# Performance work log

Hardware: AMD Instinct MI355X
Metric: run time of the kernel (lower is better)

Reference implementation:

```python
import jax, jax.numpy as jnp
import numpy as np

B, S, D = 2, 1024, 2048
L = 4
HQ, HKV, HD = 32, 8, 64
I = 5632
V = 32000
EPS = 1e-5
THETA = 10000.0
SCALE = HD ** -0.5
GROUP = HQ // HKV


def setup_inputs() -> dict:
    key = jax.random.key(0)
    ks = jax.random.split(key, 8)
    s = 0.02
    return {
        "input_ids": jax.random.randint(ks[0], (B, S), 0, V, dtype=jnp.int32),
        "positions": jnp.broadcast_to(jnp.arange(S, dtype=jnp.int32), (B, S)),
        "embed": jax.random.normal(ks[1], (V, D), jnp.float32) * s,
        "w_qkv": jax.random.normal(ks[2], (L, D, (HQ + 2 * HKV) * HD), jnp.float32) * s,
        "w_o": jax.random.normal(ks[3], (L, HQ * HD, D), jnp.float32) * s,
        "w_gate_up": jax.random.normal(ks[4], (L, D, 2 * I), jnp.float32) * s,
        "w_down": jax.random.normal(ks[5], (L, I, D), jnp.float32) * s,
        "ln1_w": jnp.ones((L, D), jnp.float32),
        "ln2_w": jnp.ones((L, D), jnp.float32),
        "norm_w": jnp.ones((D,), jnp.float32),
    }


def rmsnorm(x, w):
    var = jnp.mean(x * x, axis=-1, keepdims=True)
    return x * jax.lax.rsqrt(var + EPS) * w


def rope(positions, x):
    # x: [B, S, H, HD]; neox-style rotate-half RoPE
    inv_freq = 1.0 / (THETA ** (jnp.arange(0, HD, 2, dtype=jnp.float32) / HD))
    ang = positions.astype(jnp.float32)[..., None] * inv_freq  # [B, S, HD/2]
    cos = jnp.cos(ang)[:, :, None, :]
    sin = jnp.sin(ang)[:, :, None, :]
    x1, x2 = jnp.split(x, 2, axis=-1)
    return jnp.concatenate([x1 * cos - x2 * sin, x2 * cos + x1 * sin], axis=-1)


def llama_forward(input_ids, positions, embed, w_qkv, w_o, w_gate_up, w_down,
                  ln1_w, ln2_w, norm_w):
    h = embed[input_ids]                      # [B, S, D]
    res = jnp.zeros_like(h)
    causal = jnp.tril(jnp.ones((S, S), dtype=bool))
    neg = jnp.asarray(jnp.finfo(h.dtype).min, h.dtype)

    def layer(carry, params):
        h, res = carry
        wqkv, wo, wgu, wd, l1, l2 = params
        # fused RMSNorm + residual-add (vllm RMSNorm(x, residual) semantics)
        res = h + res
        h = rmsnorm(res, l1)
        # QKV projection + RoPE
        qkv = h @ wqkv
        q, k, v = jnp.split(qkv, [HQ * HD, (HQ + HKV) * HD], axis=-1)
        q = q.reshape(B, S, HQ, HD)
        k = k.reshape(B, S, HKV, HD)
        v = v.reshape(B, S, HKV, HD)
        q = rope(positions, q)
        k = rope(positions, k)
        # GQA: broadcast kv heads across query groups
        k = jnp.repeat(k, GROUP, axis=2)      # [B, S, HQ, HD]
        v = jnp.repeat(v, GROUP, axis=2)
        scores = jnp.einsum('bqhd,bkhd->bhqk', q, k) * SCALE
        scores = jnp.where(causal, scores, neg)
        attn = jax.nn.softmax(scores, axis=-1)
        o = jnp.einsum('bhqk,bkhd->bqhd', attn, v).reshape(B, S, HQ * HD)
        h = o @ wo
        # post-attention fused RMSNorm + residual
        res = h + res
        h = rmsnorm(res, l2)
        # SwiGLU MLP
        gu = h @ wgu
        g, u = jnp.split(gu, 2, axis=-1)
        h = (jax.nn.silu(g) * u) @ wd
        return (h, res), None

    (h, res), _ = jax.lax.scan(layer, (h, res),
                               (w_qkv, w_o, w_gate_up, w_down, ln1_w, ln2_w))
    return rmsnorm(h + res, norm_w)


def reference(input_ids, positions, embed, w_qkv, w_o, w_gate_up, w_down,
              ln1_w, ln2_w, norm_w):
    return llama_forward(input_ids, positions, embed, w_qkv, w_o, w_gate_up,
                         w_down, ln1_w, ln2_w, norm_w)
```

## Files before the change

### kernel.cpp

```cpp
#include <hip/hip_runtime.h>
#include <hip/hip_bf16.h>

#define B_ 2
#define S_ 1024
#define T_ (B_*S_)
#define D_ 2048
#define L_ 4
#define HQ_ 32
#define HKV_ 8
#define HD_ 64
#define I_ 5632
#define EPS_ 1e-5f
#define SCALE_ 0.125f

typedef __attribute__((ext_vector_type(4))) float  float4v;
typedef __attribute__((ext_vector_type(8))) short  short8v;

#define GLOAD16(g, l) \
  __builtin_amdgcn_global_load_lds((const __attribute__((address_space(1))) void*)(g), \
                                   (__attribute__((address_space(3))) void*)(l), 16, 0, 0)

__device__ __forceinline__ short f2bf(float f) {
  union { float f; unsigned u; } c; c.f = f;
  unsigned u = c.u + 0x7fffu + ((c.u >> 16) & 1u);
  return (short)(u >> 16);
}

__device__ __forceinline__ void xcd_swizzle(int gx, int gy, int& bx, int& by) {
  int nwg = gx * gy;
  int orig = by * gx + bx;
  int q = nwg >> 3, r = nwg & 7;
  int xcd = orig & 7, loc = orig >> 3;
  int swz = (xcd < r ? xcd * (q + 1) : r * (q + 1) + (xcd - r) * q) + loc;
  bx = swz / gy;
  by = swz - bx * gy;
}

__global__ __launch_bounds__(256)
void transpose_bf16(const float* __restrict__ in, short* __restrict__ out,
                    int K, int N) {
  __shared__ float t[32][33];
  const int bx = blockIdx.x * 32;
  const int by = blockIdx.y * 32;
  const int tx = threadIdx.x, ty = threadIdx.y;
  #pragma unroll
  for (int j = 0; j < 32; j += 8)
    t[ty + j][tx] = in[(size_t)(by + ty + j) * N + bx + tx];
  __syncthreads();
  #pragma unroll
  for (int j = 0; j < 32; j += 8)
    out[(size_t)(bx + ty + j) * K + by + tx] = f2bf(t[tx][ty + j]);
}

__global__ __launch_bounds__(256)
void embed_gather(const int* __restrict__ ids, const float* __restrict__ embed,
                  float* __restrict__ h) {
  size_t i = (size_t)blockIdx.x * 256 + threadIdx.x;
  int t  = (int)(i >> 9);
  int d4 = (int)(i & 511);
  ((float4v*)h)[i] = ((const float4v*)(embed + (size_t)ids[t] * D_))[d4];
}

__global__ __launch_bounds__(256)
void rmsnorm_add(const float* __restrict__ x, float* __restrict__ res,
                 const float* __restrict__ w, void* __restrict__ outp,
                 int first, int bf16out) {
  const int row = blockIdx.x;
  const int tid = threadIdx.x;
  const size_t base = (size_t)row * D_;
  float4v v0 = ((const float4v*)(x + base))[tid * 2];
  float4v v1 = ((const float4v*)(x + base))[tid * 2 + 1];
  if (!first) {
    v0 += ((const float4v*)(res + base))[tid * 2];
    v1 += ((const float4v*)(res + base))[tid * 2 + 1];
  }
  ((float4v*)(res + base))[tid * 2]     = v0;
  ((float4v*)(res + base))[tid * 2 + 1] = v1;
  float ss = v0[0]*v0[0] + v0[1]*v0[1] + v0[2]*v0[2] + v0[3]*v0[3]
           + v1[0]*v1[0] + v1[1]*v1[1] + v1[2]*v1[2] + v1[3]*v1[3];
  #pragma unroll
  for (int off = 32; off > 0; off >>= 1) ss += __shfl_xor(ss, off, 64);
  __shared__ float red[4];
  if ((tid & 63) == 0) red[tid >> 6] = ss;
  __syncthreads();
  float tot = red[0] + red[1] + red[2] + red[3];
  float rs = rsqrtf(tot * (1.0f / D_) + EPS_);
  float4v w0 = ((const float4v*)w)[tid * 2];
  float4v w1 = ((const float4v*)w)[tid * 2 + 1];
  float4v o0 = v0 * rs * w0;
  float4v o1 = v1 * rs * w1;
  if (bf16out) {
    short8v y;
    #pragma unroll
    for (int k = 0; k < 4; k++) { y[k] = f2bf(o0[k]); y[k + 4] = f2bf(o1[k]); }
    ((short8v*)((char*)outp + base * 2))[tid] = y;
  } else {
    float* op = (float*)outp + base;
    ((float4v*)op)[tid * 2]     = o0;
    ((float4v*)op)[tid * 2 + 1] = o1;
  }
}

#define BM 128
#define BN 128
#define BKS 32

__global__ __launch_bounds__(256)
void gemm_n64(const short* __restrict__ A, const short* __restrict__ Bt,
              float* __restrict__ C, int M, int N, int K) {
  __shared__ short sA[BM * BKS];
  __shared__ short sB[64 * BKS];
  int bx = blockIdx.x, by = blockIdx.y;
  xcd_swizzle(gridDim.x, gridDim.y, bx, by);
  const int tid  = threadIdx.x;
  const int lane = tid & 63;
  const int wave = tid >> 6;
  const int wm = (wave >> 1) << 6;
  const int wn = (wave & 1) << 5;
  const int row0 = by * BM;
  const int col0 = bx * 64;
  const int fr = lane & 15;
  const int fk = (lane >> 4) << 3;
  float4v acc[4][2] = {};

  const int r_st  = tid >> 2;
  const int kc_st = (tid & 3) << 3;
  const short* pA = A  + (size_t)(row0 + r_st) * K + kc_st;
  const short* pB = Bt + (size_t)(col0 + r_st) * K + kc_st;
  const size_t stride64 = (size_t)64 * K;
  short* lA0 = &sA[tid * 8];
  short* lA1 = &sA[(256 + tid) * 8];
  short* lB0 = &sB[tid * 8];

  for (int k0 = 0; k0 < K; k0 += BKS) {
    GLOAD16(pA, lA0);
    GLOAD16(pA + stride64, lA1);
    GLOAD16(pB, lB0);
    pA += BKS; pB += BKS;
    __syncthreads();
    short8v af[4], bfr[2];
    #pragma unroll
    for (int f = 0; f < 4; f++)
      af[f] = *(const short8v*)(&sA[(wm + f * 16 + fr) * BKS + fk]);
    #pragma unroll
    for (int f = 0; f < 2; f++)
      bfr[f] = *(const short8v*)(&sB[(wn + f * 16 + fr) * BKS + fk]);
    #pragma unroll
    for (int i = 0; i < 4; i++)
      #pragma unroll
      for (int j = 0; j < 2; j++)
        acc[i][j] = __builtin_amdgcn_mfma_f32_16x16x32_bf16(af[i], bfr[j], acc[i][j], 0, 0, 0);
    __syncthreads();
  }
  const int cr = (lane >> 4) << 2;
  const int cc = lane & 15;
  #pragma unroll
  for (int i = 0; i < 4; i++)
    #pragma unroll
    for (int j = 0; j < 2; j++) {
      size_t base = (size_t)(row0 + wm + i * 16 + cr) * N + col0 + wn + j * 16 + cc;
      #pragma unroll
      for (int r = 0; r < 4; r++)
        C[base + (size_t)r * N] = acc[i][j][r];
    }
}

__global__ __launch_bounds__(256)
void gemm_glu(const short* __restrict__ A, const short* __restrict__ Bt,
              short* __restrict__ mlp, int K) {
  __shared__ short sA[BM * BKS];
  __shared__ short sG[64 * BKS];
  __shared__ short sU[64 * BKS];
  int bx = blockIdx.x, by = blockIdx.y;
  xcd_swizzle(gridDim.x, gridDim.y, bx, by);
  const int tid  = threadIdx.x;
  const int lane = tid & 63;
  const int wave = tid >> 6;
  const int wm = (wave >> 1) << 6;
  const int wn = (wave & 1) << 5;
  const int row0 = by * BM;
  const int col0 = bx * 64;
  const int fr = lane & 15;
  const int fk = (lane >> 4) << 3;
  float4v accg[4][2] = {};
  float4v accu[4][2] = {};

  const int r_st  = tid >> 2;
  const int kc_st = (tid & 3) << 3;
  const short* pA = A  + (size_t)(row0 + r_st) * K + kc_st;
  const short* pG = Bt + (size_t)(col0 + r_st) * K + kc_st;
  const short* pU = Bt + (size_t)(col0 + I_ + r_st) * K + kc_st;
  const size_t stride64 = (size_t)64 * K;
  short* lA0 = &sA[tid * 8];
  short* lA1 = &sA[(256 + tid) * 8];
  short* lG0 = &sG[tid * 8];
  short* lU0 = &sU[tid * 8];

  for (int k0 = 0; k0 < K; k0 += BKS) {
    GLOAD16(pA, lA0);
    GLOAD16(pA + stride64, lA1);
    GLOAD16(pG, lG0);
    GLOAD16(pU, lU0);
    pA += BKS; pG += BKS; pU += BKS;
    __syncthreads();
    short8v af[4], bg[2], bu[2];
    #pragma unroll
    for (int f = 0; f < 4; f++)
      af[f] = *(const short8v*)(&sA[(wm + f * 16 + fr) * BKS + fk]);
    #pragma unroll
    for (int f = 0; f < 2; f++) {
      bg[f] = *(const short8v*)(&sG[(wn + f * 16 + fr) * BKS + fk]);
      bu[f] = *(const short8v*)(&sU[(wn + f * 16 + fr) * BKS + fk]);
    }
    #pragma unroll
    for (int i = 0; i < 4; i++)
      #pragma unroll
      for (int j = 0; j < 2; j++) {
        accg[i][j] = __builtin_amdgcn_mfma_f32_16x16x32_bf16(af[i], bg[j], accg[i][j], 0, 0, 0);
        accu[i][j] = __builtin_amdgcn_mfma_f32_16x16x32_bf16(af[i], bu[j], accu[i][j], 0, 0, 0);
      }
    __syncthreads();
  }
  const int cr = (lane >> 4) << 2;
  const int cc = lane & 15;
  #pragma unroll
  for (int i = 0; i < 4; i++)
    #pragma unroll
    for (int j = 0; j < 2; j++) {
      size_t base = (size_t)(row0 + wm + i * 16 + cr) * I_ + col0 + wn + j * 16 + cc;
      #pragma unroll
      for (int r = 0; r < 4; r++) {
        float g = accg[i][j][r], u = accu[i][j][r];
        mlp[base + (size_t)r * I_] = f2bf(g / (1.0f + __expf(-g)) * u);
      }
    }
}

__global__ __launch_bounds__(256)
void gemm_qkv_rope(const short* __restrict__ A, const short* __restrict__ Bt,
                   const float* __restrict__ tab, short* __restrict__ qbf,
                   short* __restrict__ kbf, short* __restrict__ vbf, int K) {
  __shared__ short sA[BM * BKS];
  __shared__ short sB[BN * BKS];
  int bx = blockIdx.x, by = blockIdx.y;
  xcd_swizzle(gridDim.x, gridDim.y, bx, by);
  const int tid  = threadIdx.x;
  const int lane = tid & 63;
  const int wave = tid >> 6;
  const int wm = (wave >> 1) << 6;
  const int wn = (wave & 1) << 6;
  const int row0 = by * BM;
  const int col0 = bx * BN;
  const int fr = lane & 15;
  const int fk = (lane >> 4) << 3;
  float4v acc[4][4] = {};

  const int r_st  = tid >> 2;
  const int kc_st = (tid & 3) << 3;
  const short* pA = A  + (size_t)(row0 + r_st) * K + kc_st;
  const short* pB = Bt + (size_t)(col0 + r_st) * K + kc_st;
  const size_t stride64 = (size_t)64 * K;
  short* lA0 = &sA[tid * 8];
  short* lA1 = &sA[(256 + tid) * 8];
  short* lB0 = &sB[tid * 8];
  short* lB1 = &sB[(256 + tid) * 8];

  for (int k0 = 0; k0 < K; k0 += BKS) {
    GLOAD16(pA, lA0);
    GLOAD16(pA + stride64, lA1);
    GLOAD16(pB, lB0);
    GLOAD16(pB + stride64, lB1);
    pA += BKS; pB += BKS;
    __syncthreads();
    short8v af[4], bfr[4];
    #pragma unroll
    for (int f = 0; f < 4; f++) {
      af[f]  = *(const short8v*)(&sA[(wm + f * 16 + fr) * BKS + fk]);
      bfr[f] = *(const short8v*)(&sB[(wn + f * 16 + fr) * BKS + fk]);
    }
    #pragma unroll
    for (int i = 0; i < 4; i++)
      #pragma unroll
      for (int j = 0; j < 4; j++)
        acc[i][j] = __builtin_amdgcn_mfma_f32_16x16x32_bf16(af[i], bfr[j], acc[i][j], 0, 0, 0);
    __syncthreads();
  }
  const int cr = (lane >> 4) << 2;
  const int cc = lane & 15;
  const int head = (col0 + wn) >> 6;

  if (head < HQ_ + HKV_) {
    const float sc = (head < HQ_) ? SCALE_ : 1.0f;
    #pragma unroll
    for (int i = 0; i < 4; i++)
      #pragma unroll
      for (int jj = 0; jj < 2; jj++)
        #pragma unroll
        for (int r = 0; r < 4; r++) {
          int m = row0 + wm + i * 16 + cr + r;
          int b = m >> 10, s = m & (S_ - 1);
          int d1 = jj * 16 + cc;
          float x1 = acc[i][jj][r], x2 = acc[i][jj + 2][r];
          const float* tb = tab + (size_t)m * 64 + d1 * 2;
          float c = tb[0], sn = tb[1];
          short y1 = f2bf((x1 * c - x2 * sn) * sc);
          short y2 = f2bf((x2 * c + x1 * sn) * sc);
          size_t base;
          if (head < HQ_)
            base = ((size_t)((b * HQ_ + head) * S_ + s)) * HD_;
          else
            base = ((size_t)((b * HKV_ + head - HQ_) * S_ + s)) * HD_;
          short* dst = (head < HQ_) ? qbf : kbf;
          dst[base + d1]      = y1;
          dst[base + d1 + 32] = y2;
        }
  } else {
    const int vh = head - HQ_ - HKV_;
    #pragma unroll
    for (int i = 0; i < 4; i++)
      #pragma unroll
      for (int j = 0; j < 4; j++)
        #pragma unroll
        for (int r = 0; r < 4; r++) {
          int m = row0 + wm + i * 16 + cr + r;
          int b = m >> 10, s = m & (S_ - 1);
          vbf[((size_t)((b * HKV_ + vh) * S_ + s)) * HD_ + j * 16 + cc] =
              f2bf(acc[i][j][r]);
        }
  }
}

__global__ __launch_bounds__(256)
void rope_table(const int* __restrict__ pos, float* __restrict__ tab) {
  int i = blockIdx.x * 256 + threadIdx.x;
  int t = i >> 5, ii = i & 31;
  float p = (float)pos[t];
  float freq = __expf(-(float)ii * (9.210340371976184f / 32.0f));
  float ang = p * freq;
  tab[2 * i]     = cosf(ang);
  tab[2 * i + 1] = sinf(ang);
}

#define KPAD 68

__global__ __launch_bounds__(256)
void transpose_v(const short* __restrict__ vbf, short* __restrict__ vtbf) {
  __shared__ short sv[64 * KPAD];
  const int jt = blockIdx.x, kh = blockIdx.y, b = blockIdx.z;
  const int tid = threadIdx.x;
  const short* src = vbf + ((size_t)((b * HKV_ + kh) * S_ + jt * 64)) * HD_;
  #pragma unroll
  for (int it = 0; it < 2; it++) {
    int c = it * 256 + tid;
    int rr = c >> 3, ch = (c & 7) * 8;
    *(short8v*)(&sv[rr * KPAD + ch]) = *(const short8v*)(src + (size_t)rr * HD_ + ch);
  }
  __syncthreads();
  const int dc = tid >> 2;
  const int jc = (tid & 3) * 16;
  short8v o1, o2;
  #pragma unroll
  for (int k = 0; k < 8; k++) o1[k] = sv[(jc + k) * KPAD + dc];
  #pragma unroll
  for (int k = 0; k < 8; k++) o2[k] = sv[(jc + 8 + k) * KPAD + dc];
  short* od = vtbf + ((size_t)((b * HKV_ + kh) * HD_ + dc)) * S_ + jt * 64 + jc;
  *(short8v*)od       = o1;
  *(short8v*)(od + 8) = o2;
}

__global__ __launch_bounds__(256)
void attn_mfma(const short* __restrict__ qbf, const short* __restrict__ kbf,
               const short* __restrict__ vtbf, short* __restrict__ obf) {
  __shared__ short sK[64 * KPAD];
  __shared__ short sVt[64 * KPAD];
  __shared__ short sP[4][16 * KPAD];
  const int qb = blockIdx.x;
  const int h  = blockIdx.y;
  const int b  = blockIdx.z;
  const int kh = h >> 2;
  const int tid  = threadIdx.x;
  const int lane = tid & 63;
  const int wv   = tid >> 6;
  const int q0 = qb * 64;
  const int cc = lane & 15;
  const int g  = lane >> 4;

  short8v qf0, qf1;
  {
    const short* qrow = qbf + ((size_t)((b * HQ_ + h) * S_ + q0 + wv * 16 + cc)) * HD_;
    qf0 = *(const short8v*)(qrow + g * 8);
    qf1 = *(const short8v*)(qrow + g * 8 + 32);
  }
  float4v accO[4] = {};
  float m_r[4], l_r[4];
  #pragma unroll
  for (int r = 0; r < 4; r++) { m_r[r] = -1e30f; l_r[r] = 0.f; }

  const short* kb = kbf  + ((size_t)(b * HKV_ + kh)) * S_ * HD_;
  const short* vb = vtbf + ((size_t)(b * HKV_ + kh)) * HD_ * S_;

  for (int jt = 0; jt <= qb; jt++) {
    const int j0 = jt * 64;
    #pragma unroll
    for (int it = 0; it < 2; it++) {
      int idx = it * 256 + tid;
      int rr = idx >> 3, ch = (idx & 7) * 8;
      *(short8v*)(&sK[rr * KPAD + ch])  = *(const short8v*)(kb + (size_t)(j0 + rr) * HD_ + ch);
      *(short8v*)(&sVt[rr * KPAD + ch]) = *(const short8v*)(vb + (size_t)rr * S_ + j0 + ch);
    }
    __syncthreads();

    float4v sc[4] = {};
    #pragma unroll
    for (int ct = 0; ct < 4; ct++) {
      short8v k0 = *(const short8v*)(&sK[(ct * 16 + cc) * KPAD + g * 8]);
      short8v k1 = *(const short8v*)(&sK[(ct * 16 + cc) * KPAD + g * 8 + 32]);
      sc[ct] = __builtin_amdgcn_mfma_f32_16x16x32_bf16(qf0, k0, sc[ct], 0, 0, 0);
      sc[ct] = __builtin_amdgcn_mfma_f32_16x16x32_bf16(qf1, k1, sc[ct], 0, 0, 0);
    }
    if (jt == qb) {
      #pragma unroll
      for (int ct = 0; ct < 4; ct++)
        #pragma unroll
        for (int r = 0; r < 4; r++)
          if (j0 + ct * 16 + cc > q0 + wv * 16 + g * 4 + r) sc[ct][r] = -1e30f;
    }
    float corr[4];
    #pragma unroll
    for (int r = 0; r < 4; r++) {
      float pm = fmaxf(fmaxf(sc[0][r], sc[1][r]), fmaxf(sc[2][r], sc[3][r]));
      pm = fmaxf(pm, __shfl_xor(pm, 1, 64));
      pm = fmaxf(pm, __shfl_xor(pm, 2, 64));
      pm = fmaxf(pm, __shfl_xor(pm, 4, 64));
      pm = fmaxf(pm, __shfl_xor(pm, 8, 64));
      float mn = fmaxf(m_r[r], pm);
      corr[r] = __expf(m_r[r] - mn);
      m_r[r] = mn;
      float rs = 0.f;
      #pragma unroll
      for (int ct = 0; ct < 4; ct++) {
        float p = __expf(sc[ct][r] - mn);
        sc[ct][r] = p;
        rs += p;
      }
      rs += __shfl_xor(rs, 1, 64);
      rs += __shfl_xor(rs, 2, 64);
      rs += __shfl_xor(rs, 4, 64);
      rs += __shfl_xor(rs, 8, 64);
      l_r[r] = l_r[r] * corr[r] + rs;
    }
    #pragma unroll
    for (int ct = 0; ct < 4; ct++)
      #pragma unroll
      for (int r = 0; r < 4; r++)
        sP[wv][(g * 4 + r) * KPAD + ct * 16 + cc] = f2bf(sc[ct][r]);
    #pragma unroll
    for (int dt = 0; dt < 4; dt++)
      #pragma unroll
      for (int r = 0; r < 4; r++)
        accO[dt][r] *= corr[r];
    short8v pf0 = *(const short8v*)(&sP[wv][cc * KPAD + g * 8]);
    short8v pf1 = *(const short8v*)(&sP[wv][cc * KPAD + g * 8 + 32]);
    #pragma unroll
    for (int dt = 0; dt < 4; dt++) {
      short8v v0 = *(const short8v*)(&sVt[(dt * 16 + cc) * KPAD + g * 8]);
      short8v v1 = *(const short8v*)(&sVt[(dt * 16 + cc) * KPAD + g * 8 + 32]);
      accO[dt] = __builtin_amdgcn_mfma_f32_16x16x32_bf16(pf0, v0, accO[dt], 0, 0, 0);
      accO[dt] = __builtin_amdgcn_mfma_f32_16x16x32_bf16(pf1, v1, accO[dt], 0, 0, 0);
    }
    __syncthreads();
  }
  #pragma unroll
  for (int dt = 0; dt < 4; dt++)
    #pragma unroll
    for (int r = 0; r < 4; r++) {
      int q = q0 + wv * 16 + g * 4 + r;
      obf[((size_t)(b * S_ + q)) * 2048 + h * 64 + dt * 16 + cc] = f2bf(accO[dt][r] / l_r[r]);
    }
}

extern "C" void kernel_launch(void* const* d_in, const int* in_sizes, int n_in,
                              void* d_out, int out_size, void* d_ws, size_t ws_size,
                              hipStream_t stream) {
  const int*   ids   = (const int*)d_in[0];
  const int*   pos   = (const int*)d_in[1];
  const float* embed = (const float*)d_in[2];
  const float* w_qkv = (const float*)d_in[3];
  const float* w_o   = (const float*)d_in[4];
  const float* w_gu  = (const float*)d_in[5];
  const float* w_dn  = (const float*)d_in[6];
  const float* ln1   = (const float*)d_in[7];
  const float* ln2   = (const float*)d_in[8];
  const float* normw = (const float*)d_in[9];
  float* out = (float*)d_out;

  char* p = (char*)d_ws;
  short* wT    = (short*)p; p += (size_t)11264 * 2048 * 2;
  float* h     = (float*)p; p += (size_t)T_ * D_ * 4;
  float* res   = (float*)p; p += (size_t)T_ * D_ * 4;
  short* hnbf  = (short*)p; p += (size_t)T_ * D_ * 2;
  short* obf   = (short*)p; p += (size_t)T_ * D_ * 2;
  short* mlpbf = (short*)p; p += (size_t)T_ * I_ * 2;
  float* tab   = (float*)p; p += (size_t)T_ * 64 * 4;
  short* qbf   = (short*)p; p += (size_t)B_ * HQ_ * S_ * HD_ * 2;
  short* kbf   = (short*)p; p += (size_t)B_ * HKV_ * S_ * HD_ * 2;
  short* vbf   = (short*)p; p += (size_t)B_ * HKV_ * S_ * HD_ * 2;
  short* vtbf  = (short*)p; p += (size_t)B_ * HKV_ * HD_ * S_ * 2;

  dim3 tb(32, 8);
  embed_gather<<<T_ * D_ / 4 / 256, 256, 0, stream>>>(ids, embed, h);
  rope_table<<<T_ * 32 / 256, 256, 0, stream>>>(pos, tab);

  for (int l = 0; l < L_; l++) {
    rmsnorm_add<<<T_, 256, 0, stream>>>(h, res, ln1 + l * D_, hnbf, l == 0 ? 1 : 0, 1);

    transpose_bf16<<<dim3(3072 / 32, 2048 / 32), tb, 0, stream>>>(
        w_qkv + (size_t)l * 2048 * 3072, wT, 2048, 3072);
    gemm_qkv_rope<<<dim3(3072 / BN, T_ / BM), 256, 0, stream>>>(
        hnbf, wT, tab, qbf, kbf, vbf, 2048);

    transpose_v<<<dim3(16, 8, 2), 256, 0, stream>>>(vbf, vtbf);
    attn_mfma<<<dim3(16, 32, 2), 256, 0, stream>>>(qbf, kbf, vtbf, obf);

    transpose_bf16<<<dim3(2048 / 32, 2048 / 32), tb, 0, stream>>>(
        w_o + (size_t)l * 2048 * 2048, wT, 2048, 2048);
    gemm_n64<<<dim3(2048 / 64, T_ / BM), 256, 0, stream>>>(
        obf, wT, h, T_, 2048, 2048);

    rmsnorm_add<<<T_, 256, 0, stream>>>(h, res, ln2 + l * D_, hnbf, 0, 1);

    transpose_bf16<<<dim3(11264 / 32, 2048 / 32), tb, 0, stream>>>(
        w_gu + (size_t)l * 2048 * 11264, wT, 2048, 11264);
    gemm_glu<<<dim3(I_ / 64, T_ / BM), 256, 0, stream>>>(
        hnbf, wT, mlpbf, 2048);

    transpose_bf16<<<dim3(2048 / 32, 5632 / 32), tb, 0, stream>>>(
        w_dn + (size_t)l * 5632 * 2048, wT, 5632, 2048);
    gemm_n64<<<dim3(2048 / 64, T_ / BM), 256, 0, stream>>>(
        mlpbf, wT, h, T_, 2048, 5632);
  }
  rmsnorm_add<<<T_, 256, 0, stream>>>(h, res, normw, out, 0, 0);
}
```

Measured before the change: 1.939 ms.

## Replace fused GLU GEMM with large-tile pipelined GEMM plus separate SwiGLU; vectorize transpose

```diff
diff --git a/kernel.cpp b/kernel.cpp
--- a/kernel.cpp
+++ b/kernel.cpp
@@ -39,17 +39,28 @@
 __global__ __launch_bounds__(256)
 void transpose_bf16(const float* __restrict__ in, short* __restrict__ out,
                     int K, int N) {
-  __shared__ float t[32][33];
-  const int bx = blockIdx.x * 32;
-  const int by = blockIdx.y * 32;
-  const int tx = threadIdx.x, ty = threadIdx.y;
-  #pragma unroll
-  for (int j = 0; j < 32; j += 8)
-    t[ty + j][tx] = in[(size_t)(by + ty + j) * N + bx + tx];
+  __shared__ float t[64][65];
+  const int bx = blockIdx.x * 64;
+  const int by = blockIdx.y * 64;
+  const int tid = threadIdx.x;
+  const int lr = tid >> 4;
+  const int lc = (tid & 15) * 4;
+  #pragma unroll
+  for (int j = 0; j < 64; j += 16) {
+    float4v v = *(const float4v*)(in + (size_t)(by + lr + j) * N + bx + lc);
+    t[lr + j][lc] = v[0]; t[lr + j][lc + 1] = v[1];
+    t[lr + j][lc + 2] = v[2]; t[lr + j][lc + 3] = v[3];
+  }
   __syncthreads();
-  #pragma unroll
-  for (int j = 0; j < 32; j += 8)
-    out[(size_t)(bx + ty + j) * K + by + tx] = f2bf(t[tx][ty + j]);
+  const int nr = tid >> 3;
+  const int kc = (tid & 7) * 8;
+  #pragma unroll
+  for (int j = 0; j < 64; j += 32) {
+    short8v y;
+    #pragma unroll
+    for (int e = 0; e < 8; e++) y[e] = f2bf(t[kc + e][nr + j]);
+    *(short8v*)(out + (size_t)(bx + nr + j) * K + by + kc) = y;
+  }
 }
 
 __global__ __launch_bounds__(256)
@@ -104,6 +115,103 @@
 #define BM 128
 #define BN 128
 #define BKS 32
+
+__global__ __launch_bounds__(512, 2)
+void gemm_big(const short* __restrict__ A, const short* __restrict__ Bt,
+              float* __restrict__ C, int M, int N, int K) {
+  __shared__ short sA[2][128 * 64];
+  __shared__ short sB[2][256 * 64];
+  int bx = blockIdx.x, by = blockIdx.y;
+  xcd_swizzle(gridDim.x, gridDim.y, bx, by);
+  const int tid  = threadIdx.x;
+  const int lane = tid & 63;
+  const int wv   = tid >> 6;
+  const int wr   = wv >> 2;
+  const int wc   = wv & 3;
+  const int row0 = by * 128;
+  const int col0 = bx * 256;
+  const int fr = lane & 15;
+  const int g  = lane >> 4;
+  const int NT = K >> 6;
+
+  float4v acc[4][4] = {};
+
+  int rA[2], cA[2], rB[4], cB[4];
+  #pragma unroll
+  for (int k = 0; k < 2; k++) {
+    int s = tid + k * 512;
+    rA[k] = s >> 3;
+    cA[k] = (((s & 7) ^ (rA[k] & 7)) << 3);
+  }
+  #pragma unroll
+  for (int k = 0; k < 4; k++) {
+    int s = tid + k * 512;
+    rB[k] = s >> 3;
+    cB[k] = (((s & 7) ^ (rB[k] & 7)) << 3);
+  }
+
+#define STAGEBIG(t, buf) do { \
+    int k0_ = (t) << 6; \
+    _Pragma("unroll") \
+    for (int k_ = 0; k_ < 2; k_++) \
+      GLOAD16(A  + (size_t)(row0 + rA[k_]) * K + k0_ + cA[k_], \
+              &sA[buf][(tid + k_ * 512) * 8]); \
+    _Pragma("unroll") \
+    for (int k_ = 0; k_ < 4; k_++) \
+      GLOAD16(Bt + (size_t)(col0 + rB[k_]) * K + k0_ + cB[k_], \
+              &sB[buf][(tid + k_ * 512) * 8]); \
+  } while (0)
+
+  STAGEBIG(0, 0);
+
+  for (int t = 0; t < NT; t++) {
+    const int cur = t & 1;
+    if (t + 1 < NT) {
+      STAGEBIG(t + 1, cur ^ 1);
+      asm volatile("s_waitcnt vmcnt(6)" ::: "memory");
+    } else {
+      asm volatile("s_waitcnt vmcnt(0)" ::: "memory");
+    }
+    __builtin_amdgcn_s_barrier();
+    __builtin_amdgcn_sched_barrier(0);
+
+    const short* pA = &sA[cur][(wr * 64) * 64];
+    const short* pB = &sB[cur][(wc * 64) * 64];
+    #pragma unroll
+    for (int ks = 0; ks < 2; ks++) {
+      const int fswk = ((((ks << 2) | g) ^ (fr & 7)) << 3);
+      short8v bfr[4], afr[4];
+      #pragma unroll
+      for (int ni = 0; ni < 4; ni++)
+        bfr[ni] = *(const short8v*)(pB + (ni * 16 + fr) * 64 + fswk);
+      #pragma unroll
+      for (int m4 = 0; m4 < 4; m4++)
+        afr[m4] = *(const short8v*)(pA + (m4 * 16 + fr) * 64 + fswk);
+      __builtin_amdgcn_s_setprio(1);
+      #pragma unroll
+      for (int m4 = 0; m4 < 4; m4++)
+        #pragma unroll
+        for (int ni = 0; ni < 4; ni++)
+          acc[m4][ni] = __builtin_amdgcn_mfma_f32_16x16x32_bf16(
+              afr[m4], bfr[ni], acc[m4][ni], 0, 0, 0);
+      __builtin_amdgcn_s_setprio(0);
+    }
+    asm volatile("" ::: "memory");
+    __builtin_amdgcn_s_barrier();
+  }
+
+  #pragma unroll
+  for (int m4 = 0; m4 < 4; m4++)
+    #pragma unroll
+    for (int ni = 0; ni < 4; ni++) {
+      size_t base = (size_t)(row0 + wr * 64 + m4 * 16 + g * 4) * N
+                    + col0 + wc * 64 + ni * 16 + fr;
+      #pragma unroll
+      for (int r = 0; r < 4; r++)
+        C[base + (size_t)r * N] = acc[m4][ni][r];
+    }
+#undef STAGEBIG
+}
 
 __global__ __launch_bounds__(256)
 void gemm_n64(const short* __restrict__ A, const short* __restrict__ Bt,
@@ -162,77 +270,6 @@
       #pragma unroll
       for (int r = 0; r < 4; r++)
         C[base + (size_t)r * N] = acc[i][j][r];
-    }
-}
-
-__global__ __launch_bounds__(256)
-void gemm_glu(const short* __restrict__ A, const short* __restrict__ Bt,
-              short* __restrict__ mlp, int K) {
-  __shared__ short sA[BM * BKS];
-  __shared__ short sG[64 * BKS];
-  __shared__ short sU[64 * BKS];
-  int bx = blockIdx.x, by = blockIdx.y;
-  xcd_swizzle(gridDim.x, gridDim.y, bx, by);
-  const int tid  = threadIdx.x;
-  const int lane = tid & 63;
-  const int wave = tid >> 6;
-  const int wm = (wave >> 1) << 6;
-  const int wn = (wave & 1) << 5;
-  const int row0 = by * BM;
-  const int col0 = bx * 64;
-  const int fr = lane & 15;
-  const int fk = (lane >> 4) << 3;
-  float4v accg[4][2] = {};
-  float4v accu[4][2] = {};
-
-  const int r_st  = tid >> 2;
-  const int kc_st = (tid & 3) << 3;
-  const short* pA = A  + (size_t)(row0 + r_st) * K + kc_st;
-  const short* pG = Bt + (size_t)(col0 + r_st) * K + kc_st;
-  const short* pU = Bt + (size_t)(col0 + I_ + r_st) * K + kc_st;
-  const size_t stride64 = (size_t)64 * K;
-  short* lA0 = &sA[tid * 8];
-  short* lA1 = &sA[(256 + tid) * 8];
-  short* lG0 = &sG[tid * 8];
-  short* lU0 = &sU[tid * 8];
-
-  for (int k0 = 0; k0 < K; k0 += BKS) {
-    GLOAD16(pA, lA0);
-    GLOAD16(pA + stride64, lA1);
-    GLOAD16(pG, lG0);
-    GLOAD16(pU, lU0);
-    pA += BKS; pG += BKS; pU += BKS;
-    __syncthreads();
-    short8v af[4], bg[2], bu[2];
-    #pragma unroll
-    for (int f = 0; f < 4; f++)
-      af[f] = *(const short8v*)(&sA[(wm + f * 16 + fr) * BKS + fk]);
-    #pragma unroll
-    for (int f = 0; f < 2; f++) {
-      bg[f] = *(const short8v*)(&sG[(wn + f * 16 + fr) * BKS + fk]);
-      bu[f] = *(const short8v*)(&sU[(wn + f * 16 + fr) * BKS + fk]);
-    }
-    #pragma unroll
-    for (int i = 0; i < 4; i++)
-      #pragma unroll
-      for (int j = 0; j < 2; j++) {
-        accg[i][j] = __builtin_amdgcn_mfma_f32_16x16x32_bf16(af[i], bg[j], accg[i][j], 0, 0, 0);
-        accu[i][j] = __builtin_amdgcn_mfma_f32_16x16x32_bf16(af[i], bu[j], accu[i][j], 0, 0, 0);
-      }
-    __syncthreads();
-  }
-  const int cr = (lane >> 4) << 2;
-  const int cc = lane & 15;
-  #pragma unroll
-  for (int i = 0; i < 4; i++)
-    #pragma unroll
-    for (int j = 0; j < 2; j++) {
-      size_t base = (size_t)(row0 + wm + i * 16 + cr) * I_ + col0 + wn + j * 16 + cc;
-      #pragma unroll
-      for (int r = 0; r < 4; r++) {
-        float g = accg[i][j][r], u = accu[i][j][r];
-        mlp[base + (size_t)r * I_] = f2bf(g / (1.0f + __expf(-g)) * u);
-      }
     }
 }
 
@@ -331,6 +368,24 @@
 }
 
 __global__ __launch_bounds__(256)
+void swiglu_kernel(const float* __restrict__ gu, short* __restrict__ mlp) {
+  size_t i = (size_t)blockIdx.x * 256 + threadIdx.x;
+  size_t t = i / 704;
+  int c = (int)(i - t * 704);
+  const float* gp = gu + t * 11264 + c * 8;
+  const float* up = gp + 5632;
+  float4v g0 = *(const float4v*)gp, g1 = *(const float4v*)(gp + 4);
+  float4v u0 = *(const float4v*)up, u1 = *(const float4v*)(up + 4);
+  short8v r;
+  #pragma unroll
+  for (int k = 0; k < 4; k++) {
+    r[k]     = f2bf(g0[k] / (1.0f + __expf(-g0[k])) * u0[k]);
+    r[k + 4] = f2bf(g1[k] / (1.0f + __expf(-g1[k])) * u1[k]);
+  }
+  ((short8v*)mlp)[i] = r;
+}
+
+__global__ __launch_bounds__(256)
 void rope_table(const int* __restrict__ pos, float* __restrict__ tab) {
   int i = blockIdx.x * 256 + threadIdx.x;
   int t = i >> 5, ii = i & 31;
@@ -506,15 +561,15 @@
   short* kbf   = (short*)p; p += (size_t)B_ * HKV_ * S_ * HD_ * 2;
   short* vbf   = (short*)p; p += (size_t)B_ * HKV_ * S_ * HD_ * 2;
   short* vtbf  = (short*)p; p += (size_t)B_ * HKV_ * HD_ * S_ * 2;
-
-  dim3 tb(32, 8);
+  float* gu    = (float*)p; p += (size_t)T_ * 2 * I_ * 4;
+
   embed_gather<<<T_ * D_ / 4 / 256, 256, 0, stream>>>(ids, embed, h);
   rope_table<<<T_ * 32 / 256, 256, 0, stream>>>(pos, tab);
 
   for (int l = 0; l < L_; l++) {
     rmsnorm_add<<<T_, 256, 0, stream>>>(h, res, ln1 + l * D_, hnbf, l == 0 ? 1 : 0, 1);
 
-    transpose_bf16<<<dim3(3072 / 32, 2048 / 32), tb, 0, stream>>>(
+    transpose_bf16<<<dim3(3072 / 64, 2048 / 64), 256, 0, stream>>>(
         w_qkv + (size_t)l * 2048 * 3072, wT, 2048, 3072);
     gemm_qkv_rope<<<dim3(3072 / BN, T_ / BM), 256, 0, stream>>>(
         hnbf, wT, tab, qbf, kbf, vbf, 2048);
@@ -522,19 +577,21 @@
     transpose_v<<<dim3(16, 8, 2), 256, 0, stream>>>(vbf, vtbf);
     attn_mfma<<<dim3(16, 32, 2), 256, 0, stream>>>(qbf, kbf, vtbf, obf);
 
-    transpose_bf16<<<dim3(2048 / 32, 2048 / 32), tb, 0, stream>>>(
+    transpose_bf16<<<dim3(2048 / 64, 2048 / 64), 256, 0, stream>>>(
         w_o + (size_t)l * 2048 * 2048, wT, 2048, 2048);
     gemm_n64<<<dim3(2048 / 64, T_ / BM), 256, 0, stream>>>(
         obf, wT, h, T_, 2048, 2048);
 
     rmsnorm_add<<<T_, 256, 0, stream>>>(h, res, ln2 + l * D_, hnbf, 0, 1);
 
-    transpose_bf16<<<dim3(11264 / 32, 2048 / 32), tb, 0, stream>>>(
+    transpose_bf16<<<dim3(11264 / 64, 2048 / 64), 256, 0, stream>>>(
         w_gu + (size_t)l * 2048 * 11264, wT, 2048, 11264);
-    gemm_glu<<<dim3(I_ / 64, T_ / BM), 256, 0, stream>>>(
-        hnbf, wT, mlpbf, 2048);
-
-    transpose_bf16<<<dim3(2048 / 32, 5632 / 32), tb, 0, stream>>>(
+    gemm_big<<<dim3(11264 / 256, T_ / 128), 512, 0, stream>>>(
+        hnbf, wT, gu, T_, 11264, 2048);
+
+    swiglu_kernel<<<T_ * I_ / 8 / 256, 256, 0, stream>>>(gu, mlpbf);
+
+    transpose_bf16<<<dim3(2048 / 64, 5632 / 64), 256, 0, stream>>>(
         w_dn + (size_t)l * 5632 * 2048, wT, 5632, 2048);
     gemm_n64<<<dim3(2048 / 64, T_ / BM), 256, 0, stream>>>(
         mlpbf, wT, h, T_, 2048, 5632);
```

After: 2.017 ms. +4.0%, slower.
